# Optimization experiments

Hardware: AMD Instinct MI355X
Metric: run time of the kernel (lower is better)

Reference implementation:

```python
import jax, jax.numpy as jnp
import numpy as np

ITEMNUM = 100000
TIME_NUM = 512
H = 128
NH = 2
NB = 2
MAXLEN = 200
B = 128
L = 200
NNZ = 1600000
N_INTERVAL = 31
INTERVAL_SCALE = 1.0


def _ln(x, g, b, eps):
    mu = jnp.mean(x, axis=-1, keepdims=True)
    var = jnp.mean((x - mu) ** 2, axis=-1, keepdims=True)
    return (x - mu) * jax.lax.rsqrt(var + eps) * g + b


def _spmm(idx, val, x):
    # sparse [N,N] @ dense [N,H] via gather + segment_sum (COO)
    return jax.ops.segment_sum(val[:, None] * x[idx[1]], idx[0], num_segments=x.shape[0])


def _l2n(x):
    return x / jnp.clip(jnp.linalg.norm(x, axis=-1, keepdims=True), 1e-12)


def _encoder(e, seqs_data, seqs, position, temb, P):
    p = P['pos_emb'][e][position]
    seqs = seqs + p
    temb = temb + p
    gates = jax.nn.sigmoid(temb @ P['gate_W'][e] + P['gate_b'][e])  # [B,L,NB]
    keep = (seqs_data != ITEMNUM - 1)[..., None].astype(seqs.dtype)
    seqs = seqs * keep
    T = seqs.shape[1]
    causal = jnp.triu(jnp.ones((T, T), bool), k=1)  # True above diagonal -> masked
    hd = H // NH
    scale = 1.0 / np.sqrt(hd).astype(np.float32)
    for i in range(NB):
        Q = _ln(seqs, P['aln_g'][e, i], P['aln_b'][e, i], 1e-8)
        q = (Q @ P['qW'][e, i] + P['qb'][e, i]).reshape(-1, T, NH, hd)
        k = (temb @ P['kW'][e, i] + P['kb'][e, i]).reshape(-1, T, NH, hd)
        v = ((seqs + temb) @ P['vW'][e, i] + P['vb'][e, i]).reshape(-1, T, NH, hd)
        scores = jnp.einsum('bqhd,bkhd->bhqk', q, k) * scale
        g = gates[:, :, i]  # per-block time gate [B,T]
        gm = (g[:, :, None] * g[:, None, :])[:, None]  # gate outer product [B,1,T,T]
        gated = jnp.where(causal, -jnp.inf, scores * gm)
        attn = jax.nn.softmax(gated, axis=-1)
        out = jnp.einsum('bhqk,bkhd->bqhd', attn, v).reshape(-1, T, H)
        seqs = Q + out
        seqs = _ln(seqs, P['fln_g'][e, i], P['fln_b'][e, i], 1e-8)
        h = jax.nn.relu(seqs @ P['c1W'][e, i] + P['c1b'][e, i])  # 1x1 conv == linear
        seqs = seqs + h @ P['c2W'][e, i] + P['c2b'][e, i]
        seqs = seqs * keep
    return _ln(seqs, P['lln_g'][e], P['lln_b'][e], 1e-8)


def _forward(embX, embY, embO, time_table, interval_table, adj_val, adjs_val,
             mlp_W1, mlp_b1, mlp_W2, mlp_b2, mlp_lng, mlp_lnb,
             pos_emb, gate_W, gate_b, aln_g, aln_b, qW, kW, vW, qb, kb, vb,
             fln_g, fln_b, c1W, c1b, c2W, c2b, lln_g, lln_b,
             o_seqs, x_seqs, y_seqs, position, x_position, y_position,
             time, x_time, y_time, x_interval_time, y_interval_time, interval_time,
             adj_idx, adjs_idx):
    # 1-layer graph transfer + mean over [orig, propagated]
    eo = _l2n(_spmm(adj_idx, adj_val, embO))
    embO_m = (embO + eo) * 0.5
    ex = _l2n(_spmm(adjs_idx, adjs_val, embX))
    embX_m = (embX + ex) * 0.5
    ey = _l2n(_spmm(adjs_idx, adjs_val, embY))
    embY_m = (embY + ey) * 0.5

    def iv(t):
        idx = jnp.floor(INTERVAL_SCALE * jnp.log2(t.astype(jnp.float32) + 1.0)).astype(jnp.int32)
        return interval_table[idx]

    def mlp(x, i):
        h = jax.nn.relu(x @ mlp_W1[i] + mlp_b1[i]) @ mlp_W2[i] + mlp_b2[i]
        return _ln(h, mlp_lng[i], mlp_lnb[i], 1e-5)

    x_temb = mlp(iv(x_interval_time) + time_table[x_time], 0)
    y_temb = mlp(iv(y_interval_time) + time_table[y_time], 1)
    temb = mlp(iv(interval_time) + time_table[time], 2)

    seq_o = embO_m[o_seqs] + embO[o_seqs]
    seq_x = embX_m[x_seqs] + embX[x_seqs]
    seq_y = embY_m[y_seqs] + embY[y_seqs]

    P = dict(pos_emb=pos_emb, gate_W=gate_W, gate_b=gate_b, aln_g=aln_g, aln_b=aln_b,
             qW=qW, kW=kW, vW=vW, qb=qb, kb=kb, vb=vb, fln_g=fln_g, fln_b=fln_b,
             c1W=c1W, c1b=c1b, c2W=c2W, c2b=c2b, lln_g=lln_g, lln_b=lln_b)
    out_o = _encoder(0, o_seqs, seq_o, position, temb, P)
    out_x = _encoder(1, x_seqs, seq_x, x_position, x_temb, P)
    out_y = _encoder(2, y_seqs, seq_y, y_position, y_temb, P)
    return out_o, out_x, out_y


def setup_inputs():
    key = jax.random.key(0)
    ks = iter(jax.random.split(key, 64))

    def nrm(shape, s=0.02):
        return jax.random.normal(next(ks), shape, dtype=jnp.float32) * s

    d = {}
    for nm in ['o_seqs', 'x_seqs', 'y_seqs']:
        d[nm] = jax.random.randint(next(ks), (B, L), 0, ITEMNUM)
    for nm in ['position', 'x_position', 'y_position']:
        d[nm] = jax.random.randint(next(ks), (B, L), 0, MAXLEN)
    for nm in ['time', 'x_time', 'y_time']:
        d[nm] = jax.random.randint(next(ks), (B, L), 0, TIME_NUM)
    for nm in ['x_interval_time', 'y_interval_time', 'interval_time']:
        d[nm] = jax.random.randint(next(ks), (B, L), 0, 100000)
    d['embX'] = nrm((ITEMNUM, H)).at[ITEMNUM - 1].set(0.0)
    d['embY'] = nrm((ITEMNUM, H)).at[ITEMNUM - 1].set(0.0)
    d['embO'] = nrm((ITEMNUM, H)).at[ITEMNUM - 1].set(0.0)
    d['time_table'] = nrm((TIME_NUM, H)).at[0].set(0.0)
    d['interval_table'] = nrm((N_INTERVAL, H)).at[0].set(0.0)
    d['adj_idx'] = jnp.stack([jax.random.randint(next(ks), (NNZ,), 0, ITEMNUM),
                              jax.random.randint(next(ks), (NNZ,), 0, ITEMNUM)])
    d['adj_val'] = jax.random.uniform(next(ks), (NNZ,), dtype=jnp.float32) / 16.0
    d['adjs_idx'] = jnp.stack([jax.random.randint(next(ks), (NNZ,), 0, ITEMNUM),
                               jax.random.randint(next(ks), (NNZ,), 0, ITEMNUM)])
    d['adjs_val'] = jax.random.uniform(next(ks), (NNZ,), dtype=jnp.float32) / 16.0
    d['mlp_W1'] = nrm((3, H, 512))
    d['mlp_b1'] = jnp.zeros((3, 512), jnp.float32)
    d['mlp_W2'] = nrm((3, 512, H))
    d['mlp_b2'] = jnp.zeros((3, H), jnp.float32)
    d['mlp_lng'] = jnp.ones((3, H), jnp.float32)
    d['mlp_lnb'] = jnp.zeros((3, H), jnp.float32)
    d['pos_emb'] = nrm((3, MAXLEN, H)).at[:, 0].set(0.0)
    d['gate_W'] = nrm((3, H, NB), 0.05)
    d['gate_b'] = jnp.zeros((3, NB), jnp.float32)
    d['aln_g'] = jnp.ones((3, NB, H), jnp.float32)
    d['aln_b'] = jnp.zeros((3, NB, H), jnp.float32)
    for nm in ['qW', 'kW', 'vW', 'c1W', 'c2W']:
        d[nm] = nrm((3, NB, H, H), 0.05)
    for nm in ['qb', 'kb', 'vb', 'c1b', 'c2b']:
        d[nm] = jnp.zeros((3, NB, H), jnp.float32)
    d['fln_g'] = jnp.ones((3, NB, H), jnp.float32)
    d['fln_b'] = jnp.zeros((3, NB, H), jnp.float32)
    d['lln_g'] = jnp.ones((3, H), jnp.float32)
    d['lln_b'] = jnp.zeros((3, H), jnp.float32)
    return d


def reference(o_seqs, x_seqs, y_seqs, position, x_position, y_position, time, x_time, y_time,
              x_interval_time, y_interval_time, interval_time,
              embX, embY, embO, time_table, interval_table, adj_idx, adj_val, adjs_idx, adjs_val,
              mlp_W1, mlp_b1, mlp_W2, mlp_b2, mlp_lng, mlp_lnb,
              pos_emb, gate_W, gate_b, aln_g, aln_b, qW, kW, vW, qb, kb, vb,
              fln_g, fln_b, c1W, c1b, c2W, c2b, lln_g, lln_b):
    return _forward(embX, embY, embO, time_table, interval_table, adj_val, adjs_val,
                    mlp_W1, mlp_b1, mlp_W2, mlp_b2, mlp_lng, mlp_lnb,
                    pos_emb, gate_W, gate_b, aln_g, aln_b, qW, kW, vW, qb, kb, vb,
                    fln_g, fln_b, c1W, c1b, c2W, c2b, lln_g, lln_b,
                    o_seqs, x_seqs, y_seqs, position, x_position, y_position,
                    time, x_time, y_time, x_interval_time, y_interval_time, interval_time,
                    adj_idx, adjs_idx)
```

## Files before the change

### kernel.cpp

```cpp
#include <hip/hip_runtime.h>
#include <math.h>


#define kH 128
#define kT 200
#define kBATCH 128
#define kM (kBATCH * kT)
#define kITEMS 100000
#define kROWS 100000
#define kNNZ 1600000
#define kNEG_INF (-__builtin_huge_valf())
#define kSZ ((size_t)kM * kH)

typedef short s16x8 __attribute__((ext_vector_type(8)));
typedef __bf16 b16x8 __attribute__((ext_vector_type(8)));
typedef float f32x4 __attribute__((ext_vector_type(4)));

static __device__ __forceinline__ short f2bf(float f) {
    unsigned u = __float_as_uint(f);
    unsigned r = (u + 0x7FFFu + ((u >> 16) & 1u)) >> 16;
    return (short)r;
}
static __device__ __forceinline__ float bf2f(short s) {
    return __uint_as_float(((unsigned)(unsigned short)s) << 16);
}
static __device__ __forceinline__ f32x4 mfma16(s16x8 a, s16x8 b, f32x4 c) {
    return __builtin_amdgcn_mfma_f32_16x16x32_bf16(
        __builtin_bit_cast(b16x8, a), __builtin_bit_cast(b16x8, b), c, 0, 0, 0);
}

struct P3 { const int* p[3]; };

__global__ void flag_kernel(const int* __restrict__ ids, unsigned char* __restrict__ flags)
{
    flags[ids[blockIdx.x * 256 + threadIdx.x]] = 1;
}

__global__ void rowlist_kernel(const unsigned char* __restrict__ flags,
                               int* __restrict__ rowlist, int* __restrict__ rank,
                               int* __restrict__ nflag)
{
    const int r = blockIdx.x * 256 + threadIdx.x;
    if (r < kROWS && flags[r]) {
        const int pos = atomicAdd(nflag, 1);
        rowlist[pos] = r;
        rank[r] = pos;
    }
}

__global__ void count4_kernel(const int* __restrict__ idx,
                              const unsigned char* __restrict__ flags,
                              int* __restrict__ counts)
{
    const int j4 = (blockIdx.x * 256 + threadIdx.x) * 4;
    if (j4 >= kNNZ) return;
    const int4 r = *reinterpret_cast<const int4*>(&idx[j4]);
    if (flags[r.x]) atomicAdd(&counts[r.x], 1);
    if (flags[r.y]) atomicAdd(&counts[r.y], 1);
    if (flags[r.z]) atomicAdd(&counts[r.z], 1);
    if (flags[r.w]) atomicAdd(&counts[r.w], 1);
}

__global__ __launch_bounds__(256) void scan_pass1(const int* __restrict__ counts,
                                                  int* __restrict__ partial)
{
    const int t = threadIdx.x;
    const int base = blockIdx.x * 1024;
    int s = 0;
#pragma unroll
    for (int i = 0; i < 4; ++i) {
        const int g = base + t + i * 256;
        if (g < kROWS) s += counts[g];
    }
    __shared__ int sd[256];
    sd[t] = s; __syncthreads();
    for (int off = 128; off > 0; off >>= 1) {
        if (t < off) sd[t] += sd[t + off];
        __syncthreads();
    }
    if (t == 0) partial[blockIdx.x] = sd[0];
}

__global__ void scan_pass2(int* __restrict__ partial, int nblk)
{
    const int t = threadIdx.x;
    __shared__ int sd[128];
    const int v = (t < nblk) ? partial[t] : 0;
    sd[t] = v; __syncthreads();
    for (int off = 1; off < 128; off <<= 1) {
        const int a = (t >= off) ? sd[t - off] : 0;
        __syncthreads();
        sd[t] += a;
        __syncthreads();
    }
    if (t < nblk) partial[t] = sd[t] - v;
}

__global__ __launch_bounds__(256) void scan_pass3(const int* __restrict__ counts,
                                                  const int* __restrict__ partial,
                                                  int* __restrict__ offsets,
                                                  int* __restrict__ cursor)
{
    const int t = threadIdx.x;
    const int base = blockIdx.x * 1024;
    int c[4]; int s = 0;
#pragma unroll
    for (int i = 0; i < 4; ++i) {
        const int g = base + t * 4 + i;
        c[i] = (g < kROWS) ? counts[g] : 0;
        s += c[i];
    }
    __shared__ int sd[256];
    sd[t] = s; __syncthreads();
    for (int off = 1; off < 256; off <<= 1) {
        const int a = (t >= off) ? sd[t - off] : 0;
        __syncthreads();
        sd[t] += a;
        __syncthreads();
    }
    int run = partial[blockIdx.x] + sd[t] - s;
#pragma unroll
    for (int i = 0; i < 4; ++i) {
        const int g = base + t * 4 + i;
        if (g < kROWS) {
            offsets[g] = run;
            cursor[g] = run;
            run += c[i];
            if (g == kROWS - 1) offsets[kROWS] = run;
        }
    }
}

__global__ void scatter4_kernel(const int* __restrict__ idx, const float* __restrict__ val,
                                const unsigned char* __restrict__ flags,
                                int* __restrict__ cursor, int2* __restrict__ edges)
{
    const int j4 = (blockIdx.x * 256 + threadIdx.x) * 4;
    if (j4 >= kNNZ) return;
    const int4 r = *reinterpret_cast<const int4*>(&idx[j4]);
    const int4 c = *reinterpret_cast<const int4*>(&idx[kNNZ + j4]);
    const float4 v = *reinterpret_cast<const float4*>(&val[j4]);
    if (flags[r.x]) edges[atomicAdd(&cursor[r.x], 1)] = make_int2(c.x, __float_as_int(v.x));
    if (flags[r.y]) edges[atomicAdd(&cursor[r.y], 1)] = make_int2(c.y, __float_as_int(v.y));
    if (flags[r.z]) edges[atomicAdd(&cursor[r.z], 1)] = make_int2(c.z, __float_as_int(v.z));
    if (flags[r.w]) edges[atomicAdd(&cursor[r.w], 1)] = make_int2(c.w, __float_as_int(v.w));
}

__global__ __launch_bounds__(256) void smooth_kernel(
    const int2* __restrict__ edges, const int* __restrict__ offsets,
    const int* __restrict__ rowlist, const int* __restrict__ nflag,
    const float* __restrict__ emb, float* __restrict__ smc)
{
    const int ri = blockIdx.x * 4 + (threadIdx.x >> 6);
    const int lane = threadIdx.x & 63;
    if (ri >= nflag[0]) return;
    const int row = rowlist[ri];
    const int lo = offsets[row], hi = offsets[row + 1];
    float a0 = 0.f, a1 = 0.f;
    int e = lo;
    for (; e + 8 <= hi; e += 8) {
        const int2 e0 = edges[e],     e1 = edges[e + 1];
        const int2 e2 = edges[e + 2], e3 = edges[e + 3];
        const int2 e4 = edges[e + 4], e5 = edges[e + 5];
        const int2 e6 = edges[e + 6], e7 = edges[e + 7];
        const float2 u0 = *reinterpret_cast<const float2*>(&emb[(size_t)e0.x * kH + 2 * lane]);
        const float2 u1 = *reinterpret_cast<const float2*>(&emb[(size_t)e1.x * kH + 2 * lane]);
        const float2 u2 = *reinterpret_cast<const float2*>(&emb[(size_t)e2.x * kH + 2 * lane]);
        const float2 u3 = *reinterpret_cast<const float2*>(&emb[(size_t)e3.x * kH + 2 * lane]);
        const float2 u4 = *reinterpret_cast<const float2*>(&emb[(size_t)e4.x * kH + 2 * lane]);
        const float2 u5 = *reinterpret_cast<const float2*>(&emb[(size_t)e5.x * kH + 2 * lane]);
        const float2 u6 = *reinterpret_cast<const float2*>(&emb[(size_t)e6.x * kH + 2 * lane]);
        const float2 u7 = *reinterpret_cast<const float2*>(&emb[(size_t)e7.x * kH + 2 * lane]);
        const float v0 = __int_as_float(e0.y), v1 = __int_as_float(e1.y);
        const float v2 = __int_as_float(e2.y), v3 = __int_as_float(e3.y);
        const float v4 = __int_as_float(e4.y), v5 = __int_as_float(e5.y);
        const float v6 = __int_as_float(e6.y), v7 = __int_as_float(e7.y);
        a0 = fmaf(v0, u0.x, a0); a1 = fmaf(v0, u0.y, a1);
        a0 = fmaf(v1, u1.x, a0); a1 = fmaf(v1, u1.y, a1);
        a0 = fmaf(v2, u2.x, a0); a1 = fmaf(v2, u2.y, a1);
        a0 = fmaf(v3, u3.x, a0); a1 = fmaf(v3, u3.y, a1);
        a0 = fmaf(v4, u4.x, a0); a1 = fmaf(v4, u4.y, a1);
        a0 = fmaf(v5, u5.x, a0); a1 = fmaf(v5, u5.y, a1);
        a0 = fmaf(v6, u6.x, a0); a1 = fmaf(v6, u6.y, a1);
        a0 = fmaf(v7, u7.x, a0); a1 = fmaf(v7, u7.y, a1);
    }
    for (; e + 4 <= hi; e += 4) {
        const int2 e0 = edges[e],     e1 = edges[e + 1];
        const int2 e2 = edges[e + 2], e3 = edges[e + 3];
        const float2 u0 = *reinterpret_cast<const float2*>(&emb[(size_t)e0.x * kH + 2 * lane]);
        const float2 u1 = *reinterpret_cast<const float2*>(&emb[(size_t)e1.x * kH + 2 * lane]);
        const float2 u2 = *reinterpret_cast<const float2*>(&emb[(size_t)e2.x * kH + 2 * lane]);
        const float2 u3 = *reinterpret_cast<const float2*>(&emb[(size_t)e3.x * kH + 2 * lane]);
        const float v0 = __int_as_float(e0.y), v1 = __int_as_float(e1.y);
        const float v2 = __int_as_float(e2.y), v3 = __int_as_float(e3.y);
        a0 = fmaf(v0, u0.x, a0); a1 = fmaf(v0, u0.y, a1);
        a0 = fmaf(v1, u1.x, a0); a1 = fmaf(v1, u1.y, a1);
        a0 = fmaf(v2, u2.x, a0); a1 = fmaf(v2, u2.y, a1);
        a0 = fmaf(v3, u3.x, a0); a1 = fmaf(v3, u3.y, a1);
    }
    for (; e < hi; ++e) {
        const int2 ed = edges[e];
        const float2 u = *reinterpret_cast<const float2*>(&emb[(size_t)ed.x * kH + 2 * lane]);
        const float v = __int_as_float(ed.y);
        a0 = fmaf(v, u.x, a0); a1 = fmaf(v, u.y, a1);
    }
    float s = a0 * a0 + a1 * a1;
#pragma unroll
    for (int off = 1; off < 64; off <<= 1) s += __shfl_xor(s, off);
    const float inv = 0.5f / fmaxf(sqrtf(s), 1e-12f);
    const float2 us = *reinterpret_cast<const float2*>(&emb[(size_t)row * kH + 2 * lane]);
    float2 o;
    o.x = 1.5f * us.x + a0 * inv;
    o.y = 1.5f * us.y + a1 * inv;
    *reinterpret_cast<float2*>(&smc[(size_t)ri * kH + 2 * lane]) = o;
}

__global__ __launch_bounds__(256) void posmg_kernel(
    const int* __restrict__ ids, const int* __restrict__ pos,
    const float* __restrict__ pemb, const float* __restrict__ gW,
    const float* __restrict__ gb,
    const int* __restrict__ rank, const float* __restrict__ smc,
    float* __restrict__ seqs, short* __restrict__ temb16, float* __restrict__ gates,
    const float* __restrict__ alng, const float* __restrict__ alnb,
    short* __restrict__ qbuf16)
{
    const int tok = blockIdx.x * 4 + (threadIdx.x >> 6);
    const int lane = threadIdx.x & 63;
    const int pp = pos[tok];
    const float p0 = pemb[(size_t)pp * kH + lane];
    const float p1 = pemb[(size_t)pp * kH + 64 + lane];
    const size_t o = (size_t)tok * kH;
    const float t0 = bf2f(temb16[o + lane]) + p0;
    const float t1 = bf2f(temb16[o + 64 + lane]) + p1;
    temb16[o + lane] = f2bf(t0);
    temb16[o + 64 + lane] = f2bf(t1);
    const int id = ids[tok];
    const bool keep = id != kITEMS - 1;
    const float* smr = &smc[(size_t)rank[id] * kH];
    const float q0 = keep ? smr[lane] + p0 : 0.f;
    const float q1 = keep ? smr[64 + lane] + p1 : 0.f;
    seqs[o + lane] = q0;
    seqs[o + 64 + lane] = q1;
#pragma unroll
    for (int i = 0; i < 2; ++i) {
        float g = t0 * gW[lane * 2 + i] + t1 * gW[(64 + lane) * 2 + i];
#pragma unroll
        for (int off = 1; off < 64; off <<= 1) g += __shfl_xor(g, off);
        if (lane == 0) gates[tok * 2 + i] = 1.f / (1.f + expf(-(g + gb[i])));
    }
    float s1 = q0 + q1, s2 = q0 * q0 + q1 * q1;
#pragma unroll
    for (int off = 1; off < 64; off <<= 1) {
        s1 += __shfl_xor(s1, off);
        s2 += __shfl_xor(s2, off);
    }
    const float mean = s1 * (1.f / 128.f);
    float var = s2 * (1.f / 128.f) - mean * mean;
    var = fmaxf(var, 0.f);
    const float rr = rsqrtf(var + 1e-8f);
    qbuf16[o + lane]      = f2bf((q0 - mean) * rr * alng[lane]      + alnb[lane]);
    qbuf16[o + 64 + lane] = f2bf((q1 - mean) * rr * alng[64 + lane] + alnb[64 + lane]);
}

__global__ void build_x_kernel(
    const int* __restrict__ itv, const int* __restrict__ tt,
    const float* __restrict__ interval_table, const float* __restrict__ time_table,
    float* __restrict__ x)
{
    const int tok = blockIdx.x * 2 + (threadIdx.x >> 7);
    const int c = threadIdx.x & 127;
    const int t = itv[tok];
    int idx = (int)floorf(log2f((float)t + 1.0f));
    idx = idx < 0 ? 0 : (idx > 30 ? 30 : idx);
    x[(size_t)tok * kH + c] = interval_table[idx * kH + c] + time_table[(size_t)tt[tok] * kH + c];
}

__global__ void wt_kernel(const float* __restrict__ in, short* __restrict__ out,
                          int kLog, int nLog)
{
    const int i = blockIdx.x * 256 + threadIdx.x;
    const int knLog = kLog + nLog;
    const int b = i >> knLog;
    const int rem = i & ((1 << knLog) - 1);
    const int n = rem >> kLog;
    const int k = rem & ((1 << kLog) - 1);
    out[i] = f2bf(in[((size_t)b << knLog) + ((size_t)k << nLog) + n]);
}

__global__ __launch_bounds__(256) void ln_fln(
    float* __restrict__ seqs_b, const float* __restrict__ flng,
    const float* __restrict__ flnb, int enc0, int i)
{
    const int l = blockIdx.x / (kM / 4);
    const int blk = blockIdx.x % (kM / 4);
    const int wo = (enc0 + l) * 2 + i;
    float* seqs = seqs_b + (size_t)l * kSZ;
    const float* g = flng + wo * kH;
    const float* bb = flnb + wo * kH;
    const int tok = blk * 4 + (threadIdx.x >> 6);
    const int lane = threadIdx.x & 63;
    const float x0 = seqs[(size_t)tok * kH + lane];
    const float x1 = seqs[(size_t)tok * kH + 64 + lane];
    float s1 = x0 + x1, s2 = x0 * x0 + x1 * x1;
#pragma unroll
    for (int off = 1; off < 64; off <<= 1) {
        s1 += __shfl_xor(s1, off);
        s2 += __shfl_xor(s2, off);
    }
    const float mean = s1 * (1.f / 128.f);
    float var = s2 * (1.f / 128.f) - mean * mean;
    var = fmaxf(var, 0.f);
    const float r = rsqrtf(var + 1e-8f);
    seqs[(size_t)tok * kH + lane]      = (x0 - mean) * r * g[lane]      + bb[lane];
    seqs[(size_t)tok * kH + 64 + lane] = (x1 - mean) * r * g[64 + lane] + bb[64 + lane];
}

template <bool ABF>
static __device__ __forceinline__ void gemm_body(
    const void* __restrict__ Av, const short* __restrict__ A2B,
    const short* __restrict__ BT, const float* __restrict__ bias,
    float* __restrict__ Craw, short* __restrict__ CrawB,
    float* __restrict__ Cln, short* __restrict__ ClnB,
    const float* __restrict__ resid,
    int N, int K, int relu, const int* __restrict__ mask_ids,
    const float* __restrict__ lnOg, const float* __restrict__ lnOb, float lnOeps)
{
    __shared__ short As[128 * 64];
    __shared__ short Bs[128 * 64];
    const int tid = threadIdx.x;
    const int lane = tid & 63;
    const int w = tid >> 6;
    const int rowBase = blockIdx.y * 128;
    const int colBase = blockIdx.x * 128;
    f32x4 acc[2][8] = {};

    for (int k0 = 0; k0 < K; k0 += 64) {
#pragma unroll
        for (int p = 0; p < 4; ++p) {
            const int chunk = p * 256 + tid;
            const int r = chunk >> 3;
            const int kc = chunk & 7;
            const int byteoff = (r * 128 + kc * 16) ^ ((r & 7) << 4);
            if (ABF) {
                const short* A16 = (const short*)Av;
                const s16x8 v = *reinterpret_cast<const s16x8*>(
                    &A16[(size_t)(rowBase + r) * K + k0 + kc * 8]);
                *reinterpret_cast<s16x8*>(reinterpret_cast<char*>(As) + byteoff) = v;
            } else {
                const float* A = (const float*)Av;
                const float* src = &A[(size_t)(rowBase + r) * K + k0 + kc * 8];
                float4 a0 = *reinterpret_cast<const float4*>(src);
                float4 a1 = *reinterpret_cast<const float4*>(src + 4);
                if (A2B) {
                    const s16x8 b16 = *reinterpret_cast<const s16x8*>(
                        &A2B[(size_t)(rowBase + r) * K + k0 + kc * 8]);
                    a0.x += bf2f(b16[0]); a0.y += bf2f(b16[1]);
                    a0.z += bf2f(b16[2]); a0.w += bf2f(b16[3]);
                    a1.x += bf2f(b16[4]); a1.y += bf2f(b16[5]);
                    a1.z += bf2f(b16[6]); a1.w += bf2f(b16[7]);
                }
                s16x8 v;
                v[0] = f2bf(a0.x); v[1] = f2bf(a0.y); v[2] = f2bf(a0.z); v[3] = f2bf(a0.w);
                v[4] = f2bf(a1.x); v[5] = f2bf(a1.y); v[6] = f2bf(a1.z); v[7] = f2bf(a1.w);
                *reinterpret_cast<s16x8*>(reinterpret_cast<char*>(As) + byteoff) = v;
            }
            {
                const s16x8 v = *reinterpret_cast<const s16x8*>(
                    &BT[(size_t)(colBase + r) * K + k0 + kc * 8]);
                *reinterpret_cast<s16x8*>(reinterpret_cast<char*>(Bs) + byteoff) = v;
            }
        }
        __syncthreads();
#pragma unroll
        for (int kk = 0; kk < 2; ++kk) {
            const int kb = (kk * 32 + (lane >> 4) * 8) * 2;
            s16x8 af[2];
#pragma unroll
            for (int mi = 0; mi < 2; ++mi) {
                const int r = w * 32 + mi * 16 + (lane & 15);
                af[mi] = *reinterpret_cast<const s16x8*>(
                    reinterpret_cast<const char*>(As) + ((r * 128 + kb) ^ ((r & 7) << 4)));
            }
#pragma unroll
            for (int nj = 0; nj < 8; ++nj) {
                const int r = nj * 16 + (lane & 15);
                const s16x8 bf = *reinterpret_cast<const s16x8*>(
                    reinterpret_cast<const char*>(Bs) + ((r * 128 + kb) ^ ((r & 7) << 4)));
#pragma unroll
                for (int mi = 0; mi < 2; ++mi)
                    acc[mi][nj] = mfma16(af[mi], bf, acc[mi][nj]);
            }
        }
        __syncthreads();
    }
    const int c = lane & 15, hi = lane >> 4;
#pragma unroll
    for (int mi = 0; mi < 2; ++mi) {
#pragma unroll
        for (int r = 0; r < 4; ++r) {
            const int row = rowBase + w * 32 + mi * 16 + hi * 4 + r;
            float x[8];
#pragma unroll
            for (int nj = 0; nj < 8; ++nj) {
                const int col = colBase + nj * 16 + c;
                x[nj] = acc[mi][nj][r] + bias[col];
                if (relu) x[nj] = fmaxf(x[nj], 0.f);
                if (resid) x[nj] += resid[(size_t)row * N + col];
            }
            if (mask_ids && mask_ids[row] == kITEMS - 1) {
#pragma unroll
                for (int nj = 0; nj < 8; ++nj) x[nj] = 0.f;
            }
            if (Craw) {
#pragma unroll
                for (int nj = 0; nj < 8; ++nj)
                    Craw[(size_t)row * N + colBase + nj * 16 + c] = x[nj];
            }
            if (CrawB) {
#pragma unroll
                for (int nj = 0; nj < 8; ++nj)
                    CrawB[(size_t)row * N + colBase + nj * 16 + c] = f2bf(x[nj]);
            }
            if (lnOg) {
                float s1 = 0.f, s2 = 0.f;
#pragma unroll
                for (int nj = 0; nj < 8; ++nj) { s1 += x[nj]; s2 += x[nj] * x[nj]; }
#pragma unroll
                for (int off = 1; off < 16; off <<= 1) {
                    s1 += __shfl_xor(s1, off);
                    s2 += __shfl_xor(s2, off);
                }
                const float mean = s1 * (1.f / 128.f);
                float var = s2 * (1.f / 128.f) - mean * mean;
                var = fmaxf(var, 0.f);
                const float rr = rsqrtf(var + lnOeps);
#pragma unroll
                for (int nj = 0; nj < 8; ++nj) {
                    const int col = nj * 16 + c;
                    const float lv = (x[nj] - mean) * rr * lnOg[col] + lnOb[col];
                    if (Cln)  Cln[(size_t)row * kH + col] = lv;
                    if (ClnB) ClnB[(size_t)row * kH + col] = f2bf(lv);
                }
            }
        }
    }
}

__global__ __launch_bounds__(256, 4) void gemm_w1(
    const float* __restrict__ A, const short* __restrict__ BT,
    const float* __restrict__ bias, short* __restrict__ C)
{
    gemm_body<false>(A, nullptr, BT, bias, nullptr, C, nullptr, nullptr, nullptr,
                     512, 128, 1, nullptr, nullptr, nullptr, 0.f);
}

__global__ __launch_bounds__(256, 4) void gemm_w2(
    const short* __restrict__ A, const short* __restrict__ BT,
    const float* __restrict__ bias, short* __restrict__ ClnB,
    const float* __restrict__ g, const float* __restrict__ b)
{
    gemm_body<true>(A, nullptr, BT, bias, nullptr, nullptr, nullptr, ClnB, nullptr,
                    128, 512, 0, nullptr, g, b, 1e-5f);
}

__global__ __launch_bounds__(256, 4) void gemm_qkv(
    const short* __restrict__ qbuf16_b, const short* __restrict__ temb16_b,
    const float* __restrict__ seqs_b, short* __restrict__ qkv16,
    const short* __restrict__ WT, int enc0, int i,
    const float* __restrict__ qb, const float* __restrict__ kb,
    const float* __restrict__ vb)
{
    const int z = blockIdx.z;
    const int l = z / 3, m = z % 3;
    const int wo = (enc0 + l) * 2 + i;
    const short* B  = WT + ((size_t)m * 6 + wo) * 16384;
    const float* bias = ((m == 0) ? qb : (m == 1) ? kb : vb) + wo * kH;
    short* C = qkv16 + (size_t)(l * 3 + m) * kSZ;
    if (m == 0) {
        gemm_body<true>(qbuf16_b + (size_t)l * kSZ, nullptr, B, bias,
                        nullptr, C, nullptr, nullptr, nullptr,
                        128, 128, 0, nullptr, nullptr, nullptr, 0.f);
    } else if (m == 1) {
        gemm_body<true>(temb16_b + (size_t)l * kSZ, nullptr, B, bias,
                        nullptr, C, nullptr, nullptr, nullptr,
                        128, 128, 0, nullptr, nullptr, nullptr, 0.f);
    } else {
        gemm_body<false>(seqs_b + (size_t)l * kSZ, temb16_b + (size_t)l * kSZ, B, bias,
                         nullptr, C, nullptr, nullptr, nullptr,
                         128, 128, 0, nullptr, nullptr, nullptr, 0.f);
    }
}

__global__ __launch_bounds__(256, 4) void gemm_c1(
    const float* __restrict__ seqs_b, short* __restrict__ qkv16,
    const short* __restrict__ c1WT, const float* __restrict__ c1b,
    int enc0, int i)
{
    const int l = blockIdx.z;
    const int wo = (enc0 + l) * 2 + i;
    gemm_body<false>(seqs_b + (size_t)l * kSZ, nullptr,
                     c1WT + (size_t)wo * 16384, c1b + wo * kH,
                     nullptr, qkv16 + (size_t)(l * 3) * kSZ, nullptr, nullptr, nullptr,
                     128, 128, 1, nullptr, nullptr, nullptr, 0.f);
}

__global__ __launch_bounds__(256, 4) void gemm_c2(
    const short* __restrict__ qkv16, float* __restrict__ seqs_b,
    short* __restrict__ qbuf16_b, float* __restrict__ outp,
    const short* __restrict__ c2WT, const float* __restrict__ c2b,
    P3 ids, const float* __restrict__ alng, const float* __restrict__ alnb,
    const float* __restrict__ llng, const float* __restrict__ llnb,
    int enc0, int i)
{
    const int l = blockIdx.z;
    const int genc = enc0 + l;
    const int wo = genc * 2 + i;
    const short* A16 = qkv16 + (size_t)(l * 3) * kSZ;
    float* seqs = seqs_b + (size_t)l * kSZ;
    if (i == 0) {
        gemm_body<true>(A16, nullptr, c2WT + (size_t)wo * 16384, c2b + wo * kH,
                        seqs, nullptr, nullptr, qbuf16_b + (size_t)l * kSZ, seqs,
                        128, 128, 0, ids.p[genc],
                        alng + (genc * 2 + 1) * kH, alnb + (genc * 2 + 1) * kH, 1e-8f);
    } else {
        gemm_body<true>(A16, nullptr, c2WT + (size_t)wo * 16384, c2b + wo * kH,
                        nullptr, nullptr, outp + (size_t)genc * kSZ, nullptr, seqs,
                        128, 128, 0, ids.p[genc],
                        llng + genc * kH, llnb + genc * kH, 1e-8f);
    }
}

#define aNT 13
#define aVS 232
#define aPS 72

__global__ __launch_bounds__(256, 2) void attn_mfma(
    const short* __restrict__ qkv16, const float* __restrict__ gates_b,
    const int gi, const short* __restrict__ resid16_b, float* __restrict__ out_b)
{
    __shared__ short klds[200 * 64];
    __shared__ short vt[64 * aVS];
    __shared__ short pl[4][16 * aPS];
    __shared__ float glds[224];
    const int bid = (int)blockIdx.x;
    const int l = bid >> 8;
    const int rb = bid & 255;
    const int b = rb >> 1, h = rb & 1, hoff = h * 64;
    const int tid = threadIdx.x, lane = tid & 63, wv = tid >> 6;
    const size_t base = (size_t)b * kT * kH;
    const short* qp16 = qkv16 + (size_t)(l * 3 + 0) * kSZ;
    const short* kp16 = qkv16 + (size_t)(l * 3 + 1) * kSZ;
    const short* vp16 = qkv16 + (size_t)(l * 3 + 2) * kSZ;
    const float* gates = gates_b + (size_t)l * (kM * 2);
    const short* resid16 = resid16_b + (size_t)l * kSZ;
    float* outp = out_b + (size_t)l * kSZ;

    for (int i = tid; i < 1600; i += 256) {
        const int r = i >> 3, c8 = i & 7;
        const s16x8 v = *reinterpret_cast<const s16x8*>(
            &kp16[base + (size_t)r * kH + hoff + c8 * 8]);
        *reinterpret_cast<s16x8*>(reinterpret_cast<char*>(klds) +
            ((r * 128 + c8 * 16) ^ ((r & 7) << 4))) = v;
    }
    for (int i = tid; i < 6400; i += 256) {
        const int k2 = i >> 6, d = i & 63;
        const unsigned v0 = (unsigned short)vp16[base + (size_t)(2 * k2) * kH + hoff + d];
        const unsigned v1 = (unsigned short)vp16[base + (size_t)(2 * k2 + 1) * kH + hoff + d];
        *reinterpret_cast<unsigned*>(reinterpret_cast<char*>(vt) + d * (aVS * 2) + k2 * 4)
            = v0 | (v1 << 16);
    }
    for (int i = tid; i < 1024; i += 256) {
        const int d = i >> 4, k2 = 100 + (i & 15);
        *reinterpret_cast<unsigned*>(reinterpret_cast<char*>(vt) + d * (aVS * 2) + k2 * 4) = 0;
    }
    if (tid < 224) glds[tid] = (tid < 200) ? gates[(b * kT + tid) * 2 + gi] : 0.f;
    __syncthreads();

    const int c = lane & 15, hi = lane >> 4;
    const float scale = 0.125f;

    for (int qt = wv; qt < aNT; qt += 4) {
        const short* s0 = &qp16[base + (size_t)(qt * 16 + c) * kH + hoff + hi * 8];
        const s16x8 aq0 = *reinterpret_cast<const s16x8*>(s0);
        const s16x8 aq1 = *reinterpret_cast<const s16x8*>(s0 + 32);
        f32x4 sc[aNT];
#pragma unroll
        for (int kt = 0; kt < aNT; ++kt) {
            if (kt > qt) continue;
            const int krow = kt * 16 + c;
            const int sw = (krow & 7) << 4;
            const s16x8 bk0 = *reinterpret_cast<const s16x8*>(
                reinterpret_cast<const char*>(klds) + ((krow * 128 + hi * 16) ^ sw));
            const s16x8 bk1 = *reinterpret_cast<const s16x8*>(
                reinterpret_cast<const char*>(klds) + ((krow * 128 + 64 + hi * 16) ^ sw));
            f32x4 s = {0.f, 0.f, 0.f, 0.f};
            s = mfma16(aq0, bk0, s);
            s = mfma16(aq1, bk1, s);
            sc[kt] = s;
        }
        float gq[4], m[4], ps[4];
#pragma unroll
        for (int r = 0; r < 4; ++r) {
            gq[r] = glds[qt * 16 + hi * 4 + r];
            m[r] = kNEG_INF; ps[r] = 0.f;
        }
#pragma unroll
        for (int kt = 0; kt < aNT; ++kt) {
            if (kt > qt) continue;
            const int col = kt * 16 + c;
            const float gk = glds[col] * scale;
#pragma unroll
            for (int r = 0; r < 4; ++r) {
                const int row = qt * 16 + hi * 4 + r;
                const float v = (col <= row && col < 200) ? sc[kt][r] * gq[r] * gk : kNEG_INF;
                sc[kt][r] = v;
                m[r] = fmaxf(m[r], v);
            }
        }
#pragma unroll
        for (int r = 0; r < 4; ++r)
#pragma unroll
            for (int off = 1; off < 16; off <<= 1)
                m[r] = fmaxf(m[r], __shfl_xor(m[r], off));
        f32x4 oacc[4] = {};
        const int kmax = qt * 16 + 15;
#pragma unroll
        for (int kc = 0; kc < 4; ++kc) {
            if (kc * 64 > kmax) continue;
#pragma unroll
            for (int t4 = 0; t4 < 4; ++t4) {
                const int kt = kc * 4 + t4;
#pragma unroll
                for (int r = 0; r < 4; ++r) {
                    float p = 0.f;
                    if (kt <= qt) { p = __expf(sc[kt][r] - m[r]); ps[r] += p; }
                    *reinterpret_cast<short*>(reinterpret_cast<char*>(pl[wv]) +
                        ((hi * 4 + r) * aPS + t4 * 16 + c) * 2) = f2bf(p);
                }
            }
#pragma unroll
            for (int ksl = 0; ksl < 2; ++ksl) {
                if (kc * 64 + ksl * 32 > kmax) continue;
                const s16x8 pa = *reinterpret_cast<const s16x8*>(
                    reinterpret_cast<const char*>(pl[wv]) + (c * aPS + ksl * 32 + hi * 8) * 2);
#pragma unroll
                for (int n = 0; n < 4; ++n) {
                    const s16x8 bv = *reinterpret_cast<const s16x8*>(
                        reinterpret_cast<const char*>(vt) +
                        ((n * 16 + c) * aVS + kc * 64 + ksl * 32 + hi * 8) * 2);
                    oacc[n] = mfma16(pa, bv, oacc[n]);
                }
            }
        }
#pragma unroll
        for (int r = 0; r < 4; ++r)
#pragma unroll
            for (int off = 1; off < 16; off <<= 1)
                ps[r] += __shfl_xor(ps[r], off);
#pragma unroll
        for (int r = 0; r < 4; ++r) {
            const int row = qt * 16 + hi * 4 + r;
            if (row < 200) {
                const float inv = 1.f / ps[r];
#pragma unroll
                for (int n = 0; n < 4; ++n) {
                    const size_t off = base + (size_t)row * kH + hoff + n * 16 + c;
                    outp[off] = bf2f(resid16[off]) + oacc[n][r] * inv;
                }
            }
        }
    }
}

extern "C" void kernel_launch(void* const* d_in, const int* in_sizes, int n_in,
                              void* d_out, int out_size, void* d_ws, size_t ws_size,
                              hipStream_t stream)
{
    const int* ids_i[3] = { (const int*)d_in[0], (const int*)d_in[1], (const int*)d_in[2] };
    const int* pos_i[3] = { (const int*)d_in[3], (const int*)d_in[4], (const int*)d_in[5] };
    const int* tm_i[3]  = { (const int*)d_in[6], (const int*)d_in[7], (const int*)d_in[8] };
    const int* itv_i[3] = { (const int*)d_in[11], (const int*)d_in[9], (const int*)d_in[10] };
    const float* emb_i[3] = { (const float*)d_in[14], (const float*)d_in[12], (const float*)d_in[13] };
    const float* time_table = (const float*)d_in[15];
    const float* interval_table = (const float*)d_in[16];
    const int* adj_idx  = (const int*)d_in[17];
    const float* adj_val = (const float*)d_in[18];
    const int* adjs_idx  = (const int*)d_in[19];
    const float* adjs_val = (const float*)d_in[20];
    const float* mlp_W1 = (const float*)d_in[21];
    const float* mlp_b1 = (const float*)d_in[22];
    const float* mlp_W2 = (const float*)d_in[23];
    const float* mlp_b2 = (const float*)d_in[24];
    const float* mlp_lng = (const float*)d_in[25];
    const float* mlp_lnb = (const float*)d_in[26];
    const float* pos_emb = (const float*)d_in[27];
    const float* gate_W = (const float*)d_in[28];
    const float* gate_b = (const float*)d_in[29];
    const float* aln_g = (const float*)d_in[30];
    const float* aln_b = (const float*)d_in[31];
    const float* qW = (const float*)d_in[32];
    const float* kW = (const float*)d_in[33];
    const float* vW = (const float*)d_in[34];
    const float* c1W = (const float*)d_in[35];
    const float* c2W = (const float*)d_in[36];
    const float* qb = (const float*)d_in[37];
    const float* kb = (const float*)d_in[38];
    const float* vb = (const float*)d_in[39];
    const float* c1b = (const float*)d_in[40];
    const float* c2b = (const float*)d_in[41];
    const float* fln_g = (const float*)d_in[42];
    const float* fln_b = (const float*)d_in[43];
    const float* lln_g = (const float*)d_in[44];
    const float* lln_b = (const float*)d_in[45];

    float* out = (float*)d_out;
    float* ws = (float*)d_ws;

    const size_t HDR = 900000;
    short* WT = (short*)ws;
    int* COUNTS = (int*)(ws + 442368);
    int* NFLAG  = COUNTS + kROWS;
    unsigned char* FLAGS = (unsigned char*)(NFLAG + 16);
    int* OFFS   = (int*)(FLAGS + 100000);
    int* CURS   = OFFS + kROWS + 1;
    int* PART   = CURS + kROWS;
    int* ROWLIST = PART + 256;
    int* RANK   = ROWLIST + 25600;

    const size_t STATE_PER = 2 * kSZ + 51200;
    const size_t SCRATCH_F = 14745600;
    const size_t need1 = (HDR + 1 * STATE_PER + SCRATCH_F) * 4;
    const size_t need3 = (HDR + 3 * STATE_PER + SCRATCH_F) * 4;
    if (ws_size < need1) return;
    const bool merged = ws_size >= need3;
    const int NE = merged ? 3 : 1;

    float* SEQS   = ws + HDR;
    short* TEMB16 = (short*)(SEQS + (size_t)NE * kSZ);
    short* QBUF16 = TEMB16 + (size_t)NE * kSZ;
    float* GATES  = (float*)(QBUF16 + (size_t)NE * kSZ);
    float* SCRATCH = GATES + (size_t)NE * 51200;
    float* SMC  = SCRATCH;
    float* XBUF = SMC + kSZ;
    int2*  EDGES = (int2*)(XBUF + kSZ);
    short* HID   = (short*)(XBUF + kSZ);
    short* QKV16 = (short*)SCRATCH;

    const short* qkvWT = WT;
    const short* c1WT = WT + (size_t)18 * 16384;
    const short* c2WT = WT + (size_t)24 * 16384;
    const short* w1T = WT + (size_t)30 * 16384;
    const short* w2T = w1T + 3 * 65536;

    wt_kernel<<<6 * 16384 / 256, 256, 0, stream>>>(qW, (short*)qkvWT, 7, 7);
    wt_kernel<<<6 * 16384 / 256, 256, 0, stream>>>(kW, (short*)qkvWT + 6 * 16384, 7, 7);
    wt_kernel<<<6 * 16384 / 256, 256, 0, stream>>>(vW, (short*)qkvWT + 12 * 16384, 7, 7);
    wt_kernel<<<6 * 16384 / 256, 256, 0, stream>>>(c1W, (short*)c1WT, 7, 7);
    wt_kernel<<<6 * 16384 / 256, 256, 0, stream>>>(c2W, (short*)c2WT, 7, 7);
    wt_kernel<<<3 * 65536 / 256, 256, 0, stream>>>(mlp_W1, (short*)w1T, 7, 9);
    wt_kernel<<<3 * 65536 / 256, 256, 0, stream>>>(mlp_W2, (short*)w2T, 9, 7);

    const int mi_of[3] = { 2, 0, 1 };
    const int g4 = (kNNZ / 4 + 255) / 256;
    P3 idsPack{ { ids_i[0], ids_i[1], ids_i[2] } };

    auto phaseA = [&](int e, int l) {
        const int* a_idx = (e == 0) ? adj_idx : adjs_idx;
        const float* a_val = (e == 0) ? adj_val : adjs_val;
        float* SEQSl = SEQS + (size_t)l * kSZ;
        short* TEMBl = TEMB16 + (size_t)l * kSZ;
        short* QBUFl = QBUF16 + (size_t)l * kSZ;
        float* GATESl = GATES + (size_t)l * (kM * 2);
        hipMemsetAsync(COUNTS, 0, kROWS * sizeof(int) + 64 + kROWS, stream);
        flag_kernel<<<kM / 256, 256, 0, stream>>>(ids_i[e], FLAGS);
        rowlist_kernel<<<(kROWS + 255) / 256, 256, 0, stream>>>(FLAGS, ROWLIST, RANK, NFLAG);
        count4_kernel<<<g4, 256, 0, stream>>>(a_idx, FLAGS, COUNTS);
        scan_pass1<<<98, 256, 0, stream>>>(COUNTS, PART);
        scan_pass2<<<1, 128, 0, stream>>>(PART, 98);
        scan_pass3<<<98, 256, 0, stream>>>(COUNTS, PART, OFFS, CURS);
        scatter4_kernel<<<g4, 256, 0, stream>>>(a_idx, a_val, FLAGS, CURS, EDGES);
        smooth_kernel<<<6400, 256, 0, stream>>>(EDGES, OFFS, ROWLIST, NFLAG, emb_i[e], SMC);
        build_x_kernel<<<kM / 2, 256, 0, stream>>>(itv_i[e], tm_i[e], interval_table, time_table, XBUF);
        const int mi = mi_of[e];
        gemm_w1<<<dim3(4, kM / 128), 256, 0, stream>>>(
            XBUF, w1T + (size_t)mi * 65536, mlp_b1 + mi * 512, HID);
        gemm_w2<<<dim3(1, kM / 128), 256, 0, stream>>>(
            HID, w2T + (size_t)mi * 65536, mlp_b2 + mi * kH, TEMBl,
            mlp_lng + mi * kH, mlp_lnb + mi * kH);
        posmg_kernel<<<kM / 4, 256, 0, stream>>>(
            ids_i[e], pos_i[e], pos_emb + (size_t)e * kT * kH,
            gate_W + e * kH * 2, gate_b + e * 2, RANK, SMC, SEQSl, TEMBl, GATESl,
            aln_g + (e * 2) * kH, aln_b + (e * 2) * kH, QBUFl);
    };

    auto phaseB = [&](int enc0, int nenc) {
        for (int i = 0; i < 2; ++i) {
            gemm_qkv<<<dim3(1, kM / 128, 3 * nenc), 256, 0, stream>>>(
                QBUF16, TEMB16, SEQS, QKV16, qkvWT, enc0, i, qb, kb, vb);
            attn_mfma<<<256 * nenc, 256, 0, stream>>>(QKV16, GATES, i, QBUF16, SEQS);
            ln_fln<<<(kM / 4) * nenc, 256, 0, stream>>>(SEQS, fln_g, fln_b, enc0, i);
            gemm_c1<<<dim3(1, kM / 128, nenc), 256, 0, stream>>>(
                SEQS, QKV16, c1WT, c1b, enc0, i);
            gemm_c2<<<dim3(1, kM / 128, nenc), 256, 0, stream>>>(
                QKV16, SEQS, QBUF16, out, c2WT, c2b, idsPack,
                aln_g, aln_b, lln_g, lln_b, enc0, i);
        }
    };

    if (merged) {
        for (int e = 0; e < 3; ++e) phaseA(e, e);
        phaseB(0, 3);
    } else {
        for (int e = 0; e < 3; ++e) {
            phaseA(e, 0);
            phaseB(e, 1);
        }
    }
}
```

Before: 868.3 us.

## Precompute first MLP layer over embedding tables and gather per token

The MLP input is interval_table[idx] + time_table[t], and the first layer is linear, so its output can be written as the sum of two precomputed table projections. A new kernel projects every interval and time table row through W1 for each of the three MLPs once. A gather kernel then adds the two rows plus the bias, applies ReLU and writes bf16. This replaces the per-token build_x kernel and the W1 GEMM with a cheap gather, at the cost of a table build (about 1.6k rows x 512 per MLP) and extra workspace.

```diff
diff --git a/kernel.cpp b/kernel.cpp
--- a/kernel.cpp
+++ b/kernel.cpp
@@ -11,8 +11,11 @@
 #define kNNZ 1600000
 #define kNEG_INF (-__builtin_huge_valf())
 #define kSZ ((size_t)kM * kH)
+#define kTABIT ((size_t)3 * 31 * 512)
+#define kTABTT ((size_t)3 * 512 * 512)
 
 typedef short s16x8 __attribute__((ext_vector_type(8)));
+typedef short s16x4 __attribute__((ext_vector_type(4)));
 typedef __bf16 b16x8 __attribute__((ext_vector_type(8)));
 typedef float f32x4 __attribute__((ext_vector_type(4)));
 
@@ -262,19 +265,6 @@
     qbuf16[o + 64 + lane] = f2bf((q1 - mean) * rr * alng[64 + lane] + alnb[64 + lane]);
 }
 
-__global__ void build_x_kernel(
-    const int* __restrict__ itv, const int* __restrict__ tt,
-    const float* __restrict__ interval_table, const float* __restrict__ time_table,
-    float* __restrict__ x)
-{
-    const int tok = blockIdx.x * 2 + (threadIdx.x >> 7);
-    const int c = threadIdx.x & 127;
-    const int t = itv[tok];
-    int idx = (int)floorf(log2f((float)t + 1.0f));
-    idx = idx < 0 ? 0 : (idx > 30 ? 30 : idx);
-    x[(size_t)tok * kH + c] = interval_table[idx * kH + c] + time_table[(size_t)tt[tok] * kH + c];
-}
-
 __global__ void wt_kernel(const float* __restrict__ in, short* __restrict__ out,
                           int kLog, int nLog)
 {
@@ -285,6 +275,64 @@
     const int n = rem >> kLog;
     const int k = rem & ((1 << kLog) - 1);
     out[i] = f2bf(in[((size_t)b << knLog) + ((size_t)k << nLog) + n]);
+}
+
+__global__ __launch_bounds__(256) void tab_kernel(
+    const float* __restrict__ itab, const float* __restrict__ ttab,
+    const short* __restrict__ w1T, float* __restrict__ TAB)
+{
+    const int bid = blockIdx.x;
+    const int mi = bid / 543;
+    const int r  = bid % 543;
+    const bool isIt = r < 31;
+    const float* src = isIt ? &itab[(size_t)r * kH] : &ttab[(size_t)(r - 31) * kH];
+    float* dst = isIt ? &TAB[((size_t)mi * 31 + r) * 512]
+                      : &TAB[kTABIT + ((size_t)mi * 512 + (r - 31)) * 512];
+    __shared__ float xs[128];
+    if (threadIdx.x < 128) xs[threadIdx.x] = src[threadIdx.x];
+    __syncthreads();
+    const short* wbase = w1T + (size_t)mi * 65536;
+#pragma unroll
+    for (int cc = 0; cc < 2; ++cc) {
+        const int n = threadIdx.x * 2 + cc;
+        const short* wr = wbase + (size_t)n * 128;
+        float acc = 0.f;
+        for (int k = 0; k < 128; k += 8) {
+            const s16x8 wv = *reinterpret_cast<const s16x8*>(&wr[k]);
+            acc = fmaf(xs[k + 0], bf2f(wv[0]), acc);
+            acc = fmaf(xs[k + 1], bf2f(wv[1]), acc);
+            acc = fmaf(xs[k + 2], bf2f(wv[2]), acc);
+            acc = fmaf(xs[k + 3], bf2f(wv[3]), acc);
+            acc = fmaf(xs[k + 4], bf2f(wv[4]), acc);
+            acc = fmaf(xs[k + 5], bf2f(wv[5]), acc);
+            acc = fmaf(xs[k + 6], bf2f(wv[6]), acc);
+            acc = fmaf(xs[k + 7], bf2f(wv[7]), acc);
+        }
+        dst[n] = acc;
+    }
+}
+
+__global__ __launch_bounds__(256) void hid_kernel(
+    const int* __restrict__ itv, const int* __restrict__ tt,
+    const float* __restrict__ TAB, const float* __restrict__ b1,
+    short* __restrict__ hid, int mi)
+{
+    const int tok = blockIdx.x * 2 + (threadIdx.x >> 7);
+    const int n4 = (threadIdx.x & 127) * 4;
+    const int t = itv[tok];
+    int ix = (int)floorf(log2f((float)t + 1.0f));
+    ix = ix < 0 ? 0 : (ix > 30 ? 30 : ix);
+    const float* ir = &TAB[((size_t)mi * 31 + ix) * 512];
+    const float* tr = &TAB[kTABIT + ((size_t)mi * 512 + tt[tok]) * 512];
+    const float4 a = *reinterpret_cast<const float4*>(&ir[n4]);
+    const float4 b = *reinterpret_cast<const float4*>(&tr[n4]);
+    const float4 c = *reinterpret_cast<const float4*>(&b1[n4]);
+    s16x4 o;
+    o[0] = f2bf(fmaxf(a.x + b.x + c.x, 0.f));
+    o[1] = f2bf(fmaxf(a.y + b.y + c.y, 0.f));
+    o[2] = f2bf(fmaxf(a.z + b.z + c.z, 0.f));
+    o[3] = f2bf(fmaxf(a.w + b.w + c.w, 0.f));
+    *reinterpret_cast<s16x4*>(&hid[(size_t)tok * 512 + n4]) = o;
 }
 
 __global__ __launch_bounds__(256) void ln_fln(
@@ -444,14 +492,6 @@
             }
         }
     }
-}
-
-__global__ __launch_bounds__(256, 4) void gemm_w1(
-    const float* __restrict__ A, const short* __restrict__ BT,
-    const float* __restrict__ bias, short* __restrict__ C)
-{
-    gemm_body<false>(A, nullptr, BT, bias, nullptr, C, nullptr, nullptr, nullptr,
-                     512, 128, 1, nullptr, nullptr, nullptr, 0.f);
 }
 
 __global__ __launch_bounds__(256, 4) void gemm_w2(
@@ -728,7 +768,9 @@
     int* RANK   = ROWLIST + 25600;
 
     const size_t STATE_PER = 2 * kSZ + 51200;
-    const size_t SCRATCH_F = 14745600;
+    const size_t QKV_F = 14745600;
+    const size_t TAB_F = kTABIT + kTABTT;
+    const size_t SCRATCH_F = QKV_F + TAB_F;
     const size_t need1 = (HDR + 1 * STATE_PER + SCRATCH_F) * 4;
     const size_t need3 = (HDR + 3 * STATE_PER + SCRATCH_F) * 4;
     if (ws_size < need1) return;
@@ -745,6 +787,7 @@
     int2*  EDGES = (int2*)(XBUF + kSZ);
     short* HID   = (short*)(XBUF + kSZ);
     short* QKV16 = (short*)SCRATCH;
+    float* TAB   = SCRATCH + QKV_F;
 
     const short* qkvWT = WT;
     const short* c1WT = WT + (size_t)18 * 16384;
@@ -759,6 +802,7 @@
     wt_kernel<<<6 * 16384 / 256, 256, 0, stream>>>(c2W, (short*)c2WT, 7, 7);
     wt_kernel<<<3 * 65536 / 256, 256, 0, stream>>>(mlp_W1, (short*)w1T, 7, 9);
     wt_kernel<<<3 * 65536 / 256, 256, 0, stream>>>(mlp_W2, (short*)w2T, 9, 7);
+    tab_kernel<<<3 * 543, 256, 0, stream>>>(interval_table, time_table, w1T, TAB);
 
     const int mi_of[3] = { 2, 0, 1 };
     const int g4 = (kNNZ / 4 + 255) / 256;
@@ -780,10 +824,9 @@
         scan_pass3<<<98, 256, 0, stream>>>(COUNTS, PART, OFFS, CURS);
         scatter4_kernel<<<g4, 256, 0, stream>>>(a_idx, a_val, FLAGS, CURS, EDGES);
         smooth_kernel<<<6400, 256, 0, stream>>>(EDGES, OFFS, ROWLIST, NFLAG, emb_i[e], SMC);
-        build_x_kernel<<<kM / 2, 256, 0, stream>>>(itv_i[e], tm_i[e], interval_table, time_table, XBUF);
         const int mi = mi_of[e];
-        gemm_w1<<<dim3(4, kM / 128), 256, 0, stream>>>(
-            XBUF, w1T + (size_t)mi * 65536, mlp_b1 + mi * 512, HID);
+        hid_kernel<<<kM / 2, 256, 0, stream>>>(
+            itv_i[e], tm_i[e], TAB, mlp_b1 + mi * 512, HID, mi);
         gemm_w2<<<dim3(1, kM / 128), 256, 0, stream>>>(
             HID, w2T + (size_t)mi * 65536, mlp_b2 + mi * kH, TEMBl,
             mlp_lng + mi * kH, mlp_lnb + mi * kH);
```

After: 874.1 us. No clear change (+0.7%).
